# Performance work log

Hardware: AMD Instinct MI355X
Metric: run time of the kernel (lower is better)

Reference implementation:

```python
import jax, jax.numpy as jnp
import numpy as np
import math

B, Q, D = 1, 1024, 4096
H, KV, HD = 32, 8, 128
GROUP_FACTOR, LABEL_BITS, HEAVY_CONST = 8, 4, 256
ROPE_THETA = 10000.0
NEG = jnp.finfo(jnp.float32).min


def setup_inputs() -> dict:
    key = jax.random.key(0)
    ks = jax.random.split(key, 5)
    hidden_states = jax.random.normal(ks[0], (B, Q, D), jnp.float32)
    Wq = jax.random.normal(ks[1], (D, H * HD), jnp.float32) * 0.02
    Wk = jax.random.normal(ks[2], (D, KV * HD), jnp.float32) * 0.02
    Wv = jax.random.normal(ks[3], (D, KV * HD), jnp.float32) * 0.02
    Wo = jax.random.normal(ks[4], (H * HD, D), jnp.float32) * 0.02
    # additive causal mask [B,1,Q,Q]
    causal = jnp.tril(jnp.ones((Q, Q), bool))
    attention_mask = jnp.where(causal, 0.0, NEG)[None, None].astype(jnp.float32)
    position_ids = jnp.arange(Q, dtype=jnp.int64 if jax.config.jax_enable_x64 else jnp.int32)[None]
    # per-head channel permutation (sorted channel importance order)
    rng = np.random.default_rng(0)
    sorted_channel = jnp.asarray(np.stack([rng.permutation(HD) for _ in range(H)]), jnp.int32)
    return {"hidden_states": hidden_states, "attention_mask": attention_mask,
            "position_ids": position_ids, "Wq": Wq, "Wk": Wk, "Wv": Wv, "Wo": Wo,
            "sorted_channel": sorted_channel}


def pseudo_quantize(t, q_bit):
    max_quant = 2 ** q_bit - 1
    mn = jnp.min(t, axis=-1, keepdims=True)
    mx = jnp.max(t, axis=-1, keepdims=True)
    rng = mx - mn
    rng = jnp.where(rng == 0, 1.0, rng)
    scale = max_quant / rng
    quant = jnp.clip(jnp.round((t - mn) * scale), 0, max_quant)
    return quant / scale + mn


def rotate_half(x):
    x1, x2 = jnp.split(x, 2, axis=-1)
    return jnp.concatenate([-x2, x1], axis=-1)


def _forward(hidden_states, attention_mask, Wq, Wk, Wv, Wo, position_ids, sorted_channel):
    bsz, q_len, _ = hidden_states.shape
    q = (hidden_states @ Wq).reshape(bsz, q_len, H, HD).transpose(0, 2, 1, 3)   # [B,H,Q,HD]
    k = (hidden_states @ Wk).reshape(bsz, q_len, KV, HD).transpose(0, 2, 1, 3)  # [B,KV,Q,HD]
    v = (hidden_states @ Wv).reshape(bsz, q_len, KV, HD).transpose(0, 2, 1, 3)
    kv_len = q_len

    # RoPE
    inv_freq = 1.0 / (ROPE_THETA ** (jnp.arange(0, HD, 2, dtype=jnp.float32) / HD))
    freqs = position_ids.astype(jnp.float32)[..., None] * inv_freq  # [B,Q,HD/2]
    emb = jnp.concatenate([freqs, freqs], axis=-1)
    cos = jnp.cos(emb)[:, None]  # [B,1,Q,HD]
    sin = jnp.sin(emb)[:, None]
    q = q * cos + rotate_half(q) * sin
    k = k * cos + rotate_half(k) * sin
    prev_q = q  # upper_layer_embedding is None -> previous_query_states == query_states

    # GQA repeat
    groups = H // KV
    k = jnp.repeat(k, groups, axis=1)  # [B,H,K,HD]
    v = jnp.repeat(v, groups, axis=1)

    attn = jnp.einsum('bhqd,bhkd->bhqk', q, k) / math.sqrt(HD)

    # channel gather per head (sorted_channel: [H,HD] permutation)
    idx = jnp.broadcast_to(sorted_channel[None, :, None, :], q.shape)
    sq = jnp.take_along_axis(prev_q, idx, axis=-1)
    sk = jnp.take_along_axis(k, jnp.broadcast_to(sorted_channel[None, :, None, :], k.shape), axis=-1)
    outlier = HD // GROUP_FACTOR
    gq = sq[..., :outlier]
    gk = sk[..., :outlier]
    if LABEL_BITS < 16:
        gq = pseudo_quantize(gq, LABEL_BITS)
        gk = pseudo_quantize(gk, LABEL_BITS)
    gattn = jnp.einsum('bhqd,bhkd->bhqk', gq, gk) / math.sqrt(outlier)

    attn = attn + attention_mask
    gattn = gattn + attention_mask

    # keep top heavy_const positions per query by grouped score (descending)
    rank = jnp.argsort(jnp.argsort(-gattn, axis=-1), axis=-1)
    attn = jnp.where(rank < HEAVY_CONST, attn, -jnp.inf)

    w = jax.nn.softmax(attn.astype(jnp.float32), axis=-1).astype(v.dtype)
    out = jnp.einsum('bhqk,bhkd->bhqd', w, v)
    out = out.transpose(0, 2, 1, 3).reshape(bsz, q_len, H * HD)
    return out @ Wo


def reference(hidden_states, attention_mask, position_ids, Wq, Wk, Wv, Wo, sorted_channel):
    return _forward(hidden_states, attention_mask, Wq, Wk, Wv, Wo, position_ids, sorted_channel)
```

## Files before the change

kernel.cpp:

```cpp
#include <hip/hip_runtime.h>
#include <hip/hip_bf16.h>
#include <math.h>


typedef __hip_bfloat16 bf16;
typedef unsigned short ushort_t;
typedef __attribute__((ext_vector_type(8))) short short8;
typedef __attribute__((ext_vector_type(4))) float f32x4;
typedef __attribute__((ext_vector_type(4))) unsigned u32x4;

#define QL   1024
#define DM   4096
#define NH   32
#define NKV  8
#define GRP  4
#define HD   128
#define OUTL 16
#define HC   256
#define MNEG (-1.0e30f)

__device__ __forceinline__ unsigned mapf(float f) {
  unsigned u = __float_as_uint(f);
  return (u & 0x80000000u) ? ~u : (u | 0x80000000u);
}

__device__ __forceinline__ unsigned short f2bf(float x) {
  unsigned u = __float_as_uint(x);
  unsigned r = (u + 0x7FFFu + ((u >> 16) & 1u)) >> 16;
  return (unsigned short)r;
}
__device__ __forceinline__ float bf2f(unsigned short h) {
  return __uint_as_float(((unsigned)h) << 16);
}

__device__ __forceinline__ unsigned cvtpk(float a, float b) {
  unsigned r;
  asm("v_cvt_pk_bf16_f32 %0, %1, %2" : "=v"(r) : "v"(a), "v"(b));
  return r;
}

__device__ __forceinline__ void split8(const float* p, short8& h, short8& l) {
  f32x4 a = *(const f32x4*)p;
  f32x4 b = *(const f32x4*)(p + 4);
#pragma unroll
  for (int i = 0; i < 4; i++) {
    unsigned short hh = f2bf(a[i]);
    h[i] = (short)hh;
    l[i] = (short)f2bf(a[i] - bf2f(hh));
  }
#pragma unroll
  for (int i = 0; i < 4; i++) {
    unsigned short hh = f2bf(b[i]);
    h[4 + i] = (short)hh;
    l[4 + i] = (short)f2bf(b[i] - bf2f(hh));
  }
}

__device__ __forceinline__ void splitp8(const float* p, unsigned* o) {
  f32x4 a = *(const f32x4*)p;
  f32x4 b = *(const f32x4*)(p + 4);
#pragma unroll
  for (int i = 0; i < 4; i++) {
    unsigned short hh = f2bf(a[i]);
    unsigned short ll = f2bf(a[i] - bf2f(hh));
    o[i] = (unsigned)hh | ((unsigned)ll << 16);
  }
#pragma unroll
  for (int i = 0; i < 4; i++) {
    unsigned short hh = f2bf(b[i]);
    unsigned short ll = f2bf(b[i] - bf2f(hh));
    o[4 + i] = (unsigned)hh | ((unsigned)ll << 16);
  }
}

__device__ __forceinline__ int aswz(int r, int k) {
  return r * 32 + (k ^ (((r >> 1) & 3) << 3));
}

__device__ __forceinline__ void gll16(const bf16* g, bf16* l) {
  __builtin_amdgcn_global_load_lds(
      (const __attribute__((address_space(1))) void*)g,
      (__attribute__((address_space(3))) void*)l, 16, 0, 0);
}

__device__ __forceinline__ int pswz(int r, int c) {
  return r * 1024 + (c ^ ((((r & 7) ^ ((c >> 5) & 7)) & 7) << 3));
}

__device__ __forceinline__ int s4(int col) {
  return col ^ (((col >> 5) & 7) << 2);
}

__device__ __forceinline__ int dppReduce32(int v) {
  v += __builtin_amdgcn_update_dpp(0, v, 0xB1, 0xF, 0xF, true);
  v += __builtin_amdgcn_update_dpp(0, v, 0x4E, 0xF, 0xF, true);
  v += __builtin_amdgcn_update_dpp(0, v, 0x124, 0xF, 0xF, true);
  v += __builtin_amdgcn_update_dpp(0, v, 0x128, 0xF, 0xF, true);
  v += __builtin_amdgcn_ds_swizzle(v, 0x401F);
  return v;
}

__device__ __forceinline__ unsigned topkSel(unsigned (&uv)[32], int j32) {
#define TST(J, M)                                                     \
  _Pragma("unroll") for (int k2 = 0; k2 < 32; k2++) if ((k2 & (J)) == 0) { \
    unsigned tt = (uv[k2] ^ (uv[k2 + (J)] >> (J))) & (M);             \
    uv[k2] ^= tt;                                                     \
    uv[k2 + (J)] ^= (tt << (J));                                      \
  }
  TST(16, 0x0000FFFFu)
  TST(8, 0x00FF00FFu)
  TST(4, 0x0F0F0F0Fu)
  TST(2, 0x33333333u)
  TST(1, 0x55555555u)
#undef TST
  unsigned sel = 0xFFFFFFFFu;
  unsigned act = 0xFFFFFFFFu, gtm = 0u;
  int greater = 0, act_tot = QL;
  bool done = false;
#pragma unroll
  for (int p = 0; p < 32; p++) {
    if (__all(done)) break;
    if (!done) {
      const unsigned ones = act & uv[p];
      const int c = dppReduce32(__popc(ones));
      if (greater + c >= HC) {
        act = ones;
        act_tot = c;
      } else {
        greater += c;
        gtm |= ones;
        act ^= ones;
        act_tot -= c;
      }
      if (greater + act_tot == HC) {
        sel = __brev(gtm | act);
        done = true;
      }
    }
  }
  if (!done) {
    const unsigned gtmN = __brev(gtm), eqmN = __brev(act);
    const int needEq = HC - greater;
    const int eqc = __popc(eqmN);
    int pre = eqc;
#pragma unroll
    for (int dlt = 1; dlt < 32; dlt <<= 1) {
      int o = __shfl_up(pre, dlt, 32);
      if (j32 >= dlt) pre += o;
    }
    pre -= eqc;
    int take = needEq - pre;
    unsigned mm = eqmN;
    sel = gtmN;
    for (int i = 0; i < take && mm != 0u; i++) {
      unsigned b = mm & (0u - mm);
      sel |= b;
      mm ^= b;
    }
  }
  return sel;
}

__global__ __launch_bounds__(256)
void transpose_bf16_kernel(const bf16* __restrict__ src, bf16* __restrict__ dst,
                           int K, int N, long long srcBS, long long dstBS) {
  __shared__ alignas(16) unsigned short tile[64][64];
  const bf16* s = src + (size_t)blockIdx.z * srcBS;
  bf16* d = dst + (size_t)blockIdx.z * dstBS;
  const int k0 = blockIdx.y * 64, n0 = blockIdx.x * 64;
  const int t = threadIdx.x;
  {
    const int r = t >> 3;
    const int c8 = (t & 7) * 8;
    const int sw0 = ((r >> 3) & 7) * 8;
    const int sw1 = (((r + 32) >> 3) & 7) * 8;
    *(short8*)&tile[r][c8 ^ sw0] =
        *(const short8*)&s[(size_t)(k0 + r) * N + n0 + c8];
    *(short8*)&tile[r + 32][c8 ^ sw1] =
        *(const short8*)&s[(size_t)(k0 + r + 32) * N + n0 + c8];
  }
  __syncthreads();
  {
    const int kc8 = t & 7;
    const int nr = t >> 3;
    short8 v0, v1;
#pragma unroll
    for (int j = 0; j < 8; j++) {
      const int rowj = kc8 * 8 + j;
      const int swj = ((rowj >> 3) & 7) * 8;
      v0[j] = (short)tile[rowj][nr ^ swj];
      v1[j] = (short)tile[rowj][(nr + 32) ^ swj];
    }
    *(short8*)&d[(size_t)(n0 + nr) * K + k0 + kc8 * 8] = v0;
    *(short8*)&d[(size_t)(n0 + nr + 32) * K + k0 + kc8 * 8] = v1;
  }
}

__global__ __launch_bounds__(256)
void split_a_kernel(const void* __restrict__ hsv, bf16* __restrict__ Ah,
                    bf16* __restrict__ Al, const ushort_t* __restrict__ msk) {
  const bool ibf = (msk[1] != 0);
  const int gid = blockIdx.x * 256 + threadIdx.x;
  const int m = gid >> 9, c = gid & 511;
  const int cs = c ^ ((m >> 1) & 3);
  const size_t srci = (size_t)m * DM + (size_t)c * 8;
  const size_t dsti = (size_t)m * DM + (size_t)cs * 8;
  if (ibf) {
    *(short8*)&Ah[dsti] = *(const short8*)((const bf16*)hsv + srci);
  } else {
    short8 h, l;
    split8((const float*)hsv + srci, h, l);
    *(short8*)&Ah[dsti] = h;
    *(short8*)&Al[dsti] = l;
  }
}

__global__ __launch_bounds__(256)
void wsplitT_kernel(const void* __restrict__ src, int Nsrc,
                    bf16* __restrict__ dh, bf16* __restrict__ dl,
                    int n_off, int wantLo, const ushort_t* __restrict__ msk) {
  const bool ibf = (msk[1] != 0);
  __shared__ alignas(16) unsigned tile[64][64];
  const int n0 = blockIdx.x * 64;
  const int k0 = blockIdx.y * 64;
  const int t = threadIdx.x;
  {
    const int r = t >> 3, c8 = (t & 7) * 8;
    unsigned p0[8], p1[8];
    if (ibf) {
      const bf16* S = (const bf16*)src;
      short8 v0 = *(const short8*)&S[(size_t)(k0 + r) * Nsrc + n0 + c8];
      short8 v1 = *(const short8*)&S[(size_t)(k0 + r + 32) * Nsrc + n0 + c8];
#pragma unroll
      for (int i = 0; i < 8; i++) {
        p0[i] = (unsigned)(unsigned short)v0[i];
        p1[i] = (unsigned)(unsigned short)v1[i];
      }
    } else {
      const float* S = (const float*)src;
      splitp8(&S[(size_t)(k0 + r) * Nsrc + n0 + c8], p0);
      splitp8(&S[(size_t)(k0 + r + 32) * Nsrc + n0 + c8], p1);
    }
    const int sw0 = ((r >> 3) & 7) * 8;
    const int sw1 = (((r + 32) >> 3) & 7) * 8;
    *(u32x4*)&tile[r][c8 ^ sw0] = *(u32x4*)&p0[0];
    *(u32x4*)&tile[r][(c8 ^ sw0) + 4] = *(u32x4*)&p0[4];
    *(u32x4*)&tile[r + 32][c8 ^ sw1] = *(u32x4*)&p1[0];
    *(u32x4*)&tile[r + 32][(c8 ^ sw1) + 4] = *(u32x4*)&p1[4];
  }
  __syncthreads();
  {
    const int kc8 = t & 7, nr = t >> 3;
    short8 h0, l0, h1, l1;
#pragma unroll
    for (int j = 0; j < 8; j++) {
      const int rowj = kc8 * 8 + j;
      const int swj = ((rowj >> 3) & 7) * 8;
      unsigned g0 = tile[rowj][nr ^ swj];
      unsigned g1 = tile[rowj][(nr + 32) ^ swj];
      h0[j] = (short)(g0 & 0xFFFFu); l0[j] = (short)(g0 >> 16);
      h1[j] = (short)(g1 & 0xFFFFu); l1[j] = (short)(g1 >> 16);
    }
    const int na = n_off + n0 + nr, nb = na + 32;
    const int cha = (k0 >> 3) + (kc8 ^ ((na >> 1) & 3));
    const int chb = (k0 >> 3) + (kc8 ^ ((nb >> 1) & 3));
    *(short8*)&dh[(size_t)na * DM + ((size_t)cha << 3)] = h0;
    *(short8*)&dh[(size_t)nb * DM + ((size_t)chb << 3)] = h1;
    if (wantLo && !ibf) {
      *(short8*)&dl[(size_t)na * DM + ((size_t)cha << 3)] = l0;
      *(short8*)&dl[(size_t)nb * DM + ((size_t)chb << 3)] = l1;
    }
  }
}

__global__ __launch_bounds__(256)
void gemm_qkv2_kernel(const bf16* __restrict__ Ah, const bf16* __restrict__ Al,
                      const bf16* __restrict__ WhT, const bf16* __restrict__ WlT,
                      float* __restrict__ C, const ushort_t* __restrict__ msk) {
  const bool ibf = (msk[1] != 0);
  const int n0 = blockIdx.x * 128;
  const int m0 = blockIdx.y * 64;
  const bool doSplit = (n0 < 5120) && !ibf;

  __shared__ alignas(16) bf16 sAh[64 * 32];
  __shared__ alignas(16) bf16 sAl[64 * 32];
  __shared__ alignas(16) bf16 sBh[128 * 32];
  __shared__ alignas(16) bf16 sBl[128 * 32];

  const int t = threadIdx.x, lane = t & 63, wave = t >> 6;
  const int wm = (wave >> 1) * 32, wn = (wave & 1) * 64;
  const int mrow = lane & 15, kq = (lane >> 4) * 8;
  const size_t aoff = (size_t)(m0 + (t >> 2)) * DM + (size_t)(t & 3) * 8;
  const size_t boff0 = (size_t)(n0 + (t >> 2)) * DM + (size_t)(t & 3) * 8;
  const size_t boff1 = (size_t)(n0 + 64 + (t >> 2)) * DM + (size_t)(t & 3) * 8;
  bf16* lA_h = sAh + wave * 512;
  bf16* lA_l = sAl + wave * 512;
  bf16* lB0h = sBh + wave * 512;
  bf16* lB1h = sBh + 2048 + wave * 512;
  bf16* lB0l = sBl + wave * 512;
  bf16* lB1l = sBl + 2048 + wave * 512;

  f32x4 acc[2][4];
#pragma unroll
  for (int i = 0; i < 2; i++)
#pragma unroll
    for (int j = 0; j < 4; j++) acc[i][j] = (f32x4){0.f, 0.f, 0.f, 0.f};

  for (int kk = 0; kk < DM; kk += 32) {
    __syncthreads();
    gll16(Ah + aoff + kk, lA_h);
    gll16(WhT + boff0 + kk, lB0h);
    gll16(WhT + boff1 + kk, lB1h);
    if (doSplit) {
      gll16(Al + aoff + kk, lA_l);
      gll16(WlT + boff0 + kk, lB0l);
      gll16(WlT + boff1 + kk, lB1l);
    }
    __syncthreads();
    short8 afh[2], bfh[4];
#pragma unroll
    for (int i = 0; i < 2; i++)
      afh[i] = *(const short8*)&sAh[aswz(wm + i * 16 + mrow, kq)];
#pragma unroll
    for (int j = 0; j < 4; j++)
      bfh[j] = *(const short8*)&sBh[aswz(wn + j * 16 + mrow, kq)];
#pragma unroll
    for (int i = 0; i < 2; i++)
#pragma unroll
      for (int j = 0; j < 4; j++)
        acc[i][j] = __builtin_amdgcn_mfma_f32_16x16x32_bf16(afh[i], bfh[j], acc[i][j], 0, 0, 0);
    if (doSplit) {
      short8 afl[2], bfl[4];
#pragma unroll
      for (int i = 0; i < 2; i++)
        afl[i] = *(const short8*)&sAl[aswz(wm + i * 16 + mrow, kq)];
#pragma unroll
      for (int j = 0; j < 4; j++)
        bfl[j] = *(const short8*)&sBl[aswz(wn + j * 16 + mrow, kq)];
#pragma unroll
      for (int i = 0; i < 2; i++)
#pragma unroll
        for (int j = 0; j < 4; j++) {
          acc[i][j] = __builtin_amdgcn_mfma_f32_16x16x32_bf16(afh[i], bfl[j], acc[i][j], 0, 0, 0);
          acc[i][j] = __builtin_amdgcn_mfma_f32_16x16x32_bf16(afl[i], bfh[j], acc[i][j], 0, 0, 0);
        }
    }
  }
  const int rq = (lane >> 4) * 4, cn = lane & 15;
#pragma unroll
  for (int i = 0; i < 2; i++)
#pragma unroll
    for (int r = 0; r < 4; r++) {
      const size_t rowi = (size_t)(m0 + wm + i * 16 + rq + r);
#pragma unroll
      for (int j = 0; j < 4; j++)
        C[rowi * 6144 + (n0 + wn + j * 16 + cn)] = acc[i][j][r];
    }
}

__global__ __launch_bounds__(256)
void gemm_wo2_kernel(const bf16* __restrict__ Ao, const bf16* __restrict__ WoT,
                     void* __restrict__ Cv, const ushort_t* __restrict__ msk) {
  const bool ibf = (msk[1] != 0);
  __shared__ alignas(16) bf16 sA[64 * 32];
  __shared__ alignas(16) bf16 sB[128 * 32];
  const int n0 = blockIdx.x * 128;
  const int m0 = blockIdx.y * 64;
  const int t = threadIdx.x, lane = t & 63, wave = t >> 6;
  const int wm = (wave >> 1) * 32, wn = (wave & 1) * 64;
  const int mrow = lane & 15, kq = (lane >> 4) * 8;
  const size_t aoff = (size_t)(m0 + (t >> 2)) * DM + (size_t)(t & 3) * 8;
  const size_t boff0 = (size_t)(n0 + (t >> 2)) * DM + (size_t)(t & 3) * 8;
  const size_t boff1 = (size_t)(n0 + 64 + (t >> 2)) * DM + (size_t)(t & 3) * 8;
  bf16* lA = sA + wave * 512;
  bf16* lB0 = sB + wave * 512;
  bf16* lB1 = sB + 2048 + wave * 512;

  f32x4 acc[2][4];
#pragma unroll
  for (int i = 0; i < 2; i++)
#pragma unroll
    for (int j = 0; j < 4; j++) acc[i][j] = (f32x4){0.f, 0.f, 0.f, 0.f};

  for (int kk = 0; kk < DM; kk += 32) {
    __syncthreads();
    gll16(Ao + aoff + kk, lA);
    gll16(WoT + boff0 + kk, lB0);
    gll16(WoT + boff1 + kk, lB1);
    __syncthreads();
    short8 af[2], bfr[4];
#pragma unroll
    for (int i = 0; i < 2; i++)
      af[i] = *(const short8*)&sA[aswz(wm + i * 16 + mrow, kq)];
#pragma unroll
    for (int j = 0; j < 4; j++)
      bfr[j] = *(const short8*)&sB[aswz(wn + j * 16 + mrow, kq)];
#pragma unroll
    for (int i = 0; i < 2; i++)
#pragma unroll
      for (int j = 0; j < 4; j++)
        acc[i][j] = __builtin_amdgcn_mfma_f32_16x16x32_bf16(af[i], bfr[j], acc[i][j], 0, 0, 0);
  }
  const int rq = (lane >> 4) * 4, cn = lane & 15;
#pragma unroll
  for (int i = 0; i < 2; i++)
#pragma unroll
    for (int r = 0; r < 4; r++) {
      const size_t rowi = (size_t)(m0 + wm + i * 16 + rq + r);
#pragma unroll
      for (int j = 0; j < 4; j++) {
        const size_t idx = rowi * DM + (n0 + wn + j * 16 + cn);
        if (ibf)
          ((bf16*)Cv)[idx] = __float2bfloat16(acc[i][j][r]);
        else
          ((float*)Cv)[idx] = acc[i][j][r];
      }
    }
}

__global__ __launch_bounds__(128)
void rope_cs_kernel(float* __restrict__ cs, float* __restrict__ sn) {
  const int pos = blockIdx.x, d = threadIdx.x;
  const float inv = (float)(1.0 / pow(10000.0, (double)(d & 63) * (1.0 / 64.0)));
  const float ang = (float)pos * inv;
  cs[pos * HD + d] = cosf(ang);
  sn[pos * HD + d] = sinf(ang);
}

__global__ __launch_bounds__(128)
void rope_q_gq_kernel(const float* __restrict__ qkv, const int* __restrict__ sc,
                      bf16* __restrict__ qr, float* __restrict__ gq,
                      const float* __restrict__ cs, const float* __restrict__ sn) {
  const int pos = blockIdx.x, h = blockIdx.y, d = threadIdx.x;
  __shared__ float sv[HD], sr[HD];
  __shared__ float smn, smx;
  float v = qkv[(size_t)pos * 6144 + h * HD + d];
  sv[d] = v;
  __syncthreads();
  const float c = cs[pos * HD + d], s = sn[pos * HD + d];
  float rot = (d < 64) ? -sv[d + 64] : sv[d - 64];
  float r = v * c + rot * s;
  sr[d] = r;
  qr[((size_t)h * QL + pos) * HD + d] = __float2bfloat16(r);
  __syncthreads();
  if (d == 0) {
    float mn = 3.4e38f, mx = -3.4e38f;
    for (int j = 0; j < OUTL; j++) {
      float g = sr[sc[h * HD + j]];
      mn = fminf(mn, g);
      mx = fmaxf(mx, g);
    }
    smn = mn; smx = mx;
  }
  __syncthreads();
  if (d < OUTL) {
    float g = sr[sc[h * HD + d]];
    float rng = smx - smn;
    if (rng == 0.f) rng = 1.f;
    float scale = 15.0f / rng;
    float qv = rintf((g - smn) * scale);
    qv = fminf(fmaxf(qv, 0.f), 15.f);
    gq[((size_t)h * QL + pos) * OUTL + d] = qv / scale + smn;
  }
}

__global__ __launch_bounds__(128)
void rope_k_gk_kernel(const float* __restrict__ qkv, const int* __restrict__ sc,
                      bf16* __restrict__ kr, bf16* __restrict__ vrow,
                      float* __restrict__ gk,
                      const float* __restrict__ cs, const float* __restrict__ sn) {
  const int pos = blockIdx.x, kvh = blockIdx.y, d = threadIdx.x;
  __shared__ float sv[HD], sr[HD];
  __shared__ float smn[GRP], smx[GRP];
  float kv = qkv[(size_t)pos * 6144 + DM + kvh * HD + d];
  float vv = qkv[(size_t)pos * 6144 + DM + NKV * HD + kvh * HD + d];
  sv[d] = kv;
  __syncthreads();
  const float c = cs[pos * HD + d], s = sn[pos * HD + d];
  float rot = (d < 64) ? -sv[d + 64] : sv[d - 64];
  float r = kv * c + rot * s;
  sr[d] = r;
  kr[((size_t)kvh * QL + pos) * HD + d] = __float2bfloat16(r);
  vrow[((size_t)kvh * QL + pos) * HD + d] = __float2bfloat16(vv);
  __syncthreads();
  if (d < 64 && (d & 15) == 0) {
    const int g = d >> 4;
    const int h = kvh * GRP + g;
    float mn = 3.4e38f, mx = -3.4e38f;
    for (int j = 0; j < OUTL; j++) {
      float x = sr[sc[h * HD + j]];
      mn = fminf(mn, x);
      mx = fmaxf(mx, x);
    }
    smn[g] = mn; smx[g] = mx;
  }
  __syncthreads();
  if (d < 64) {
    const int g = d >> 4, j = d & 15;
    const int h = kvh * GRP + g;
    float x = sr[sc[h * HD + j]];
    float rng = smx[g] - smn[g];
    if (rng == 0.f) rng = 1.f;
    float scale = 15.0f / rng;
    float qv = rintf((x - smn[g]) * scale);
    qv = fminf(fmaxf(qv, 0.f), 15.f);
    gk[((size_t)h * QL + pos) * OUTL + j] = qv / scale + smn[g];
  }
}

__global__ __launch_bounds__(512)
void attn_kernel(const bf16* __restrict__ qr, const bf16* __restrict__ kr,
                 const bf16* __restrict__ vT, const float* __restrict__ gq,
                 const float* __restrict__ gk, bf16* __restrict__ ao) {
  const int h = blockIdx.y;
  const int xb = blockIdx.x;
  const int kvh = h >> 2;
  const int t = threadIdx.x;
  const int lane = t & 63, wave = t >> 6;
  const int mrow = lane & 15, kq = (lane >> 4) * 8;
  const int g = t >> 5, j32 = t & 31;

  __shared__ alignas(16) float sBuf[16 * 1024];
  bf16* sP = (bf16*)sBuf;
  float* sLp = sBuf + 8 * 1024;

  const float* gkh = &gk[(size_t)h * QL * OUTL];
  const bf16* krh = &kr[(size_t)kvh * QL * HD];
  const bf16* vTh = &vT[(size_t)kvh * HD * QL];
  const bf16* qrh = &qr[(size_t)h * QL * HD];

  for (int half = 0; half < 2; half++) {
    const int q0 = (half == 0) ? (63 - xb) * 16 : xb * 16;
    const int kmax = q0 + 16;
    const bool needSel = (kmax > HC);
    __syncthreads();

    unsigned sel = 0xFFFFFFFFu;
    if (needSel) {
      const int rbm = q0 + g;
      float gqr[OUTL];
      {
        const float* gqp = &gq[((size_t)h * QL + q0 + g) * OUTL];
#pragma unroll
        for (int c = 0; c < 4; c++) {
          f32x4 v = *(const f32x4*)(gqp + 4 * c);
#pragma unroll
          for (int i = 0; i < 4; i++) gqr[4 * c + i] = v[i];
        }
      }
      float* rowp = &sBuf[g * 1024];
#pragma unroll 2
      for (int kk = 0; kk < 32; kk++) {
        const int key = j32 * 32 + kk;
        float s = MNEG;
        if (key <= rbm) {
          const float* gp = gkh + (size_t)key * OUTL;
          float s2 = 0.f;
#pragma unroll
          for (int c = 0; c < 4; c++) {
            f32x4 v = *(const f32x4*)(gp + 4 * c);
#pragma unroll
            for (int i = 0; i < 4; i++) s2 += gqr[4 * c + i] * v[i];
          }
          s = s2 * 0.25f;
        }
        rowp[s4(key)] = s;
      }
      __syncthreads();

      unsigned uv[32];
      {
        const int base = j32 * 32, cz = j32 & 7;
#pragma unroll
        for (int c = 0; c < 8; c++) {
          f32x4 v = *(const f32x4*)&rowp[base + ((c ^ cz) << 2)];
#pragma unroll
          for (int i = 0; i < 4; i++) uv[4 * c + i] = mapf(v[i]);
        }
      }
      sel = topkSel(uv, j32);
      __syncthreads();
    }

    {
      short8 aq[4];
#pragma unroll
      for (int kb = 0; kb < 4; kb++)
        aq[kb] = *(const short8*)&qrh[(size_t)(q0 + mrow) * HD + kb * 32 + kq];
      const int ntmax = kmax >> 4;
      for (int nt = wave; nt < ntmax; nt += 8) {
        const int kb0 = nt * 16;
        f32x4 acc = {0.f, 0.f, 0.f, 0.f};
#pragma unroll
        for (int kb = 0; kb < 4; kb++) {
          short8 bfr = *(const short8*)&krh[(size_t)(kb0 + mrow) * HD + kb * 32 + kq];
          acc = __builtin_amdgcn_mfma_f32_16x16x32_bf16(aq[kb], bfr, acc, 0, 0, 0);
        }
        const int key = kb0 + mrow;
        const int pk = s4(key);
#pragma unroll
        for (int r = 0; r < 4; r++) {
          const int m = (lane >> 4) * 4 + r;
          float v = acc[r] * 0.08838834764831845f;
          sBuf[m * 1024 + pk] = (key <= q0 + m) ? v : MNEG;
        }
      }
    }
    __syncthreads();

    float av[32];
    {
      const int base = j32 * 32, cz = j32 & 7;
      const float* rowp = &sBuf[g * 1024];
#pragma unroll
      for (int c = 0; c < 8; c++) {
        f32x4 v = *(const f32x4*)&rowp[base + ((c ^ cz) << 2)];
#pragma unroll
        for (int i = 0; i < 4; i++) av[4 * c + i] = v[i];
      }
    }
    const int rb = q0 + g;
    float mx = MNEG;
#pragma unroll
    for (int kk = 0; kk < 32; kk++) {
      const int key = j32 * 32 + kk;
      if (((sel >> kk) & 1u) && key <= rb) mx = fmaxf(mx, av[kk]);
    }
#pragma unroll
    for (int dlt = 1; dlt < 32; dlt <<= 1)
      mx = fmaxf(mx, __shfl_xor(mx, dlt, 32));
    float ls = 0.f;
#pragma unroll
    for (int kk = 0; kk < 32; kk++) {
      const int key = j32 * 32 + kk;
      float p = 0.f;
      if (((sel >> kk) & 1u) && key <= rb) {
        float e = av[kk] - mx;
        p = (e < -80.f) ? 0.f : expf(e);
        ls += p;
      }
      av[kk] = p;
    }
#pragma unroll
    for (int dlt = 1; dlt < 32; dlt <<= 1)
      ls += __shfl_xor(ls, dlt, 32);
    __syncthreads();
    if (j32 == 0) sLp[g] = ls;
#pragma unroll
    for (int c = 0; c < 4; c++) {
      u32x4 ua;
#pragma unroll
      for (int i = 0; i < 4; i++)
        ua[i] = cvtpk(av[c * 8 + 2 * i], av[c * 8 + 2 * i + 1]);
      *(u32x4*)&sP[pswz(g, j32 * 32 + c * 8)] = ua;
    }
    __syncthreads();

    {
      const int kbmax = (kmax + 31) >> 5;
      const int d0 = wave * 16;
      f32x4 acc = {0.f, 0.f, 0.f, 0.f};
      for (int kb = 0; kb < kbmax; kb++) {
        short8 af = *(const short8*)&sP[pswz(mrow, kb * 32 + kq)];
        short8 bfr = *(const short8*)&vTh[(size_t)(d0 + mrow) * QL + kb * 32 + kq];
        acc = __builtin_amdgcn_mfma_f32_16x16x32_bf16(af, bfr, acc, 0, 0, 0);
      }
#pragma unroll
      for (int r = 0; r < 4; r++) {
        const int m = (lane >> 4) * 4 + r;
        float outv = acc[r] / sLp[m];
        const int rowm = q0 + m;
        const int col = h * HD + d0 + mrow;
        const int ch = (col >> 3) ^ ((rowm >> 1) & 3);
        ao[(size_t)rowm * DM + (ch << 3) + (col & 7)] = __float2bfloat16(outv);
      }
    }
  }
}

extern "C" void kernel_launch(void* const* d_in, const int* in_sizes, int n_in,
                              void* d_out, int out_size, void* d_ws, size_t ws_size,
                              hipStream_t stream) {
  (void)in_sizes; (void)n_in; (void)out_size; (void)ws_size;
  const void* hs = d_in[0];
  const ushort_t* msk = (const ushort_t*)d_in[1];
  const void* Wq = d_in[3];
  const void* Wk = d_in[4];
  const void* Wv = d_in[5];
  const void* Wo = d_in[6];
  const int* sc = (const int*)d_in[7];

  char* ws = (char*)d_ws;
  size_t off = 0;
  auto alloc = [&](size_t bytes) {
    char* p = ws + off;
    off += (bytes + 255) & ~(size_t)255;
    return p;
  };
  float* qkv = (float*)alloc((size_t)QL * 6144 * 4);
  bf16* ao = (bf16*)qkv;
  bf16* qr = (bf16*)alloc((size_t)NH * QL * HD * 2);
  bf16* kr = (bf16*)alloc((size_t)NKV * QL * HD * 2);
  bf16* vrow = (bf16*)alloc((size_t)NKV * QL * HD * 2);
  bf16* vT = (bf16*)alloc((size_t)NKV * HD * QL * 2);
  float* gq = (float*)alloc((size_t)NH * QL * OUTL * 4);
  float* gk = (float*)alloc((size_t)NH * QL * OUTL * 4);
  float* cst = (float*)alloc((size_t)QL * HD * 4);
  float* snt = (float*)alloc((size_t)QL * HD * 4);
  bf16* Ahs = (bf16*)alloc((size_t)QL * DM * 2);
  bf16* Als = (bf16*)alloc((size_t)QL * DM * 2);
  bf16* WhT = (bf16*)alloc((size_t)6144 * DM * 2);
  bf16* WlT = (bf16*)alloc((size_t)5120 * DM * 2);
  bf16* WoT = WhT;

  rope_cs_kernel<<<dim3(QL), 128, 0, stream>>>(cst, snt);

  split_a_kernel<<<dim3(2048), 256, 0, stream>>>(hs, Ahs, Als, msk);
  wsplitT_kernel<<<dim3(64, 64), 256, 0, stream>>>(Wq, 4096, WhT, WlT, 0, 1, msk);
  wsplitT_kernel<<<dim3(16, 64), 256, 0, stream>>>(Wk, 1024, WhT, WlT, 4096, 1, msk);
  wsplitT_kernel<<<dim3(16, 64), 256, 0, stream>>>(Wv, 1024, WhT, WlT, 5120, 0, msk);

  gemm_qkv2_kernel<<<dim3(48, 16), 256, 0, stream>>>(Ahs, Als, WhT, WlT, qkv, msk);

  rope_q_gq_kernel<<<dim3(QL, NH), 128, 0, stream>>>(qkv, sc, qr, gq, cst, snt);
  rope_k_gk_kernel<<<dim3(QL, NKV), 128, 0, stream>>>(qkv, sc, kr, vrow, gk, cst, snt);
  transpose_bf16_kernel<<<dim3(2, 16, NKV), 256, 0, stream>>>(
      vrow, vT, QL, HD, (long long)(QL * HD), (long long)(HD * QL));

  wsplitT_kernel<<<dim3(64, 64), 256, 0, stream>>>(Wo, 4096, WoT, WlT, 0, 0, msk);
  attn_kernel<<<dim3(32, NH), 512, 0, stream>>>(qr, kr, vT, gq, gk, ao);

  gemm_wo2_kernel<<<dim3(32, 16), 256, 0, stream>>>(ao, WoT, d_out, msk);
}
```

Measured before the change: 721.8 us.

## Shrink attention blocks to 8 query rows and interleave heads for KV locality

```diff
diff --git a/kernel.cpp b/kernel.cpp
--- a/kernel.cpp
+++ b/kernel.cpp
@@ -508,21 +508,23 @@
   }
 }
 
-__global__ __launch_bounds__(512)
+__global__ __launch_bounds__(256)
 void attn_kernel(const bf16* __restrict__ qr, const bf16* __restrict__ kr,
                  const bf16* __restrict__ vT, const float* __restrict__ gq,
                  const float* __restrict__ gk, bf16* __restrict__ ao) {
-  const int h = blockIdx.y;
-  const int xb = blockIdx.x;
-  const int kvh = h >> 2;
+  const int bid = blockIdx.x;
+  const int kvh = bid & 7;
+  const int rem = bid >> 3;
+  const int h = (kvh << 2) | (rem & 3);
+  const int xb = rem >> 2;
   const int t = threadIdx.x;
   const int lane = t & 63, wave = t >> 6;
   const int mrow = lane & 15, kq = (lane >> 4) * 8;
   const int g = t >> 5, j32 = t & 31;
 
-  __shared__ alignas(16) float sBuf[16 * 1024];
+  __shared__ alignas(16) float sBuf[8 * 1024];
   bf16* sP = (bf16*)sBuf;
-  float* sLp = sBuf + 8 * 1024;
+  float* sLp = &sBuf[8184];
 
   const float* gkh = &gk[(size_t)h * QL * OUTL];
   const bf16* krh = &kr[(size_t)kvh * QL * HD];
@@ -530,8 +532,8 @@
   const bf16* qrh = &qr[(size_t)h * QL * HD];
 
   for (int half = 0; half < 2; half++) {
-    const int q0 = (half == 0) ? (63 - xb) * 16 : xb * 16;
-    const int kmax = q0 + 16;
+    const int q0 = (half == 0) ? (127 - xb) * 8 : xb * 8;
+    const int kmax = q0 + 8;
     const bool needSel = (kmax > HC);
     __syncthreads();
 
@@ -548,7 +550,7 @@
           for (int i = 0; i < 4; i++) gqr[4 * c + i] = v[i];
         }
       }
-      float* rowp = &sBuf[g * 1024];
+      float* slot = &sBuf[t * 32];
 #pragma unroll 2
       for (int kk = 0; kk < 32; kk++) {
         const int key = j32 * 32 + kk;
@@ -564,20 +566,12 @@
           }
           s = s2 * 0.25f;
         }
-        rowp[s4(key)] = s;
-      }
-      __syncthreads();
-
+        slot[(kk + t) & 31] = s;
+      }
       unsigned uv[32];
-      {
-        const int base = j32 * 32, cz = j32 & 7;
-#pragma unroll
-        for (int c = 0; c < 8; c++) {
-          f32x4 v = *(const f32x4*)&rowp[base + ((c ^ cz) << 2)];
-#pragma unroll
-          for (int i = 0; i < 4; i++) uv[4 * c + i] = mapf(v[i]);
-        }
-      }
+#pragma unroll
+      for (int kk = 0; kk < 32; kk++)
+        uv[kk] = mapf(slot[(kk + t) & 31]);
       sel = topkSel(uv, j32);
       __syncthreads();
     }
@@ -586,9 +580,9 @@
       short8 aq[4];
 #pragma unroll
       for (int kb = 0; kb < 4; kb++)
-        aq[kb] = *(const short8*)&qrh[(size_t)(q0 + mrow) * HD + kb * 32 + kq];
-      const int ntmax = kmax >> 4;
-      for (int nt = wave; nt < ntmax; nt += 8) {
+        aq[kb] = *(const short8*)&qrh[(size_t)(q0 + (mrow & 7)) * HD + kb * 32 + kq];
+      const int ntmax = (kmax + 15) >> 4;
+      for (int nt = wave; nt < ntmax; nt += 4) {
         const int kb0 = nt * 16;
         f32x4 acc = {0.f, 0.f, 0.f, 0.f};
 #pragma unroll
@@ -601,8 +595,10 @@
 #pragma unroll
         for (int r = 0; r < 4; r++) {
           const int m = (lane >> 4) * 4 + r;
-          float v = acc[r] * 0.08838834764831845f;
-          sBuf[m * 1024 + pk] = (key <= q0 + m) ? v : MNEG;
+          if (m < 8) {
+            float v = acc[r] * 0.08838834764831845f;
+            sBuf[m * 1024 + pk] = (key <= q0 + m) ? v : MNEG;
+          }
         }
       }
     }
@@ -645,20 +641,22 @@
     for (int dlt = 1; dlt < 32; dlt <<= 1)
       ls += __shfl_xor(ls, dlt, 32);
     __syncthreads();
+    const int kbmax = (kmax + 31) >> 5;
     if (j32 == 0) sLp[g] = ls;
-#pragma unroll
-    for (int c = 0; c < 4; c++) {
-      u32x4 ua;
-#pragma unroll
-      for (int i = 0; i < 4; i++)
-        ua[i] = cvtpk(av[c * 8 + 2 * i], av[c * 8 + 2 * i + 1]);
-      *(u32x4*)&sP[pswz(g, j32 * 32 + c * 8)] = ua;
+    if (j32 < kbmax) {
+#pragma unroll
+      for (int c = 0; c < 4; c++) {
+        u32x4 ua;
+#pragma unroll
+        for (int i = 0; i < 4; i++)
+          ua[i] = cvtpk(av[c * 8 + 2 * i], av[c * 8 + 2 * i + 1]);
+        *(u32x4*)&sP[pswz(g, j32 * 32 + c * 8)] = ua;
+      }
     }
     __syncthreads();
 
-    {
-      const int kbmax = (kmax + 31) >> 5;
-      const int d0 = wave * 16;
+    for (int dt = wave; dt < 8; dt += 4) {
+      const int d0 = dt * 16;
       f32x4 acc = {0.f, 0.f, 0.f, 0.f};
       for (int kb = 0; kb < kbmax; kb++) {
         short8 af = *(const short8*)&sP[pswz(mrow, kb * 32 + kq)];
@@ -668,11 +666,13 @@
 #pragma unroll
       for (int r = 0; r < 4; r++) {
         const int m = (lane >> 4) * 4 + r;
-        float outv = acc[r] / sLp[m];
-        const int rowm = q0 + m;
-        const int col = h * HD + d0 + mrow;
-        const int ch = (col >> 3) ^ ((rowm >> 1) & 3);
-        ao[(size_t)rowm * DM + (ch << 3) + (col & 7)] = __float2bfloat16(outv);
+        if (m < 8) {
+          float outv = acc[r] / sLp[m];
+          const int rowm = q0 + m;
+          const int col = h * HD + d0 + mrow;
+          const int ch = (col >> 3) ^ ((rowm >> 1) & 3);
+          ao[(size_t)rowm * DM + (ch << 3) + (col & 7)] = __float2bfloat16(outv);
+        }
       }
     }
   }
@@ -728,7 +728,7 @@
       vrow, vT, QL, HD, (long long)(QL * HD), (long long)(HD * QL));
 
   wsplitT_kernel<<<dim3(64, 64), 256, 0, stream>>>(Wo, 4096, WoT, WlT, 0, 0, msk);
-  attn_kernel<<<dim3(32, NH), 512, 0, stream>>>(qr, kr, vT, gq, gk, ao);
+  attn_kernel<<<dim3(2048), 256, 0, stream>>>(qr, kr, vT, gq, gk, ao);
 
   gemm_wo2_kernel<<<dim3(32, 16), 256, 0, stream>>>(ao, WoT, d_out, msk);
 }
```

Result: no change. 728.6 us (+1.0%).
